# Kernel optimization log

Hardware: AMD Instinct MI355X
Metric: run time of the kernel (lower is better)

## Reference

```python
import jax, jax.numpy as jnp
import numpy as np


def setup_inputs() -> dict:
    key = jax.random.key(0)
    ks = jax.random.split(key, 7)
    T, B, I, H, O = 512, 64, 256, 512, 64
    std = 1.0 / np.sqrt(H)
    u = lambda k, shp: jax.random.uniform(k, shp, jnp.float32, -std, std)
    return {
        "x": jax.random.normal(ks[0], (T, B, I), jnp.float32),
        "x2h_w": u(ks[1], (3 * H, I)),
        "x2h_b": u(ks[2], (3 * H,)),
        "h2h_w": u(ks[3], (3 * H, H)),
        "h2h_b": u(ks[4], (3 * H,)),
        "fc_w": jax.random.normal(ks[5], (O, H), jnp.float32) * 0.05,
        "fc_b": jnp.zeros((O,), jnp.float32),
    }


def _gru_forward(x, x2h_w, x2h_b, h2h_w, h2h_b, fc_w, fc_b):
    T, B, _ = x.shape
    H = h2h_w.shape[1]
    # Precompute input projection for all timesteps: [T, B, 3H]
    x_proj = jnp.einsum("tbi,gi->tbg", x, x2h_w) + x2h_b

    def step(h, xp):
        h_t = h @ h2h_w.T + h2h_b  # [B, 3H]
        x_r, x_u, x_n = jnp.split(xp, 3, axis=1)
        h_r, h_u, h_n = jnp.split(h_t, 3, axis=1)
        reset = jax.nn.sigmoid(x_r + h_r)
        update = jax.nn.sigmoid(x_u + h_u)
        new = jnp.tanh(x_n + reset * h_n)
        hy = update * h + (1.0 - update) * new
        return hy, hy

    h0 = jnp.zeros((B, H), x.dtype)
    h_last, rnn_activity = jax.lax.scan(step, h0, x_proj)
    out = jnp.einsum("tbh,oh->tbo", rnn_activity, fc_w) + fc_b
    return out, rnn_activity


def reference(x, x2h_w, x2h_b, h2h_w, h2h_b, fc_w, fc_b):
    return _gru_forward(x, x2h_w, x2h_b, h2h_w, h2h_b, fc_w, fc_b)
```

## Files before the change

### kernel.cpp

```cpp
#include <hip/hip_runtime.h>
#include <cstdint>
#include <cstddef>

#define TT 512
#define BB 64
#define II 256
#define HH 512
#define GG 1536
#define OO 64
#define NWG 256
#define TAGPAD 16

__global__ __launch_bounds__(256)
void xproj_kernel(const float* __restrict__ x, const float* __restrict__ w,
                  const float* __restrict__ xb, float* __restrict__ xp)
{
    __shared__ float xs[64][68];
    __shared__ float ws[64][68];
    const int t  = blockIdx.y;
    const int g0 = blockIdx.x * 64;
    const int tid = threadIdx.x;
    const int gq = tid >> 4;
    const int bq = tid & 15;
    float acc[4][4];
#pragma unroll
    for (int j = 0; j < 4; ++j)
#pragma unroll
        for (int i = 0; i < 4; ++i) acc[j][i] = 0.f;

    for (int kc = 0; kc < 4; ++kc) {
        const int k0 = kc * 64;
        __syncthreads();
        for (int idx = tid; idx < 1024; idx += 256) {
            int r = idx >> 4, c4 = (idx & 15) * 4;
            float4 v = *(const float4*)(x + ((size_t)t * BB + r) * II + k0 + c4);
            xs[r][c4] = v.x; xs[r][c4+1] = v.y; xs[r][c4+2] = v.z; xs[r][c4+3] = v.w;
            float4 u = *(const float4*)(w + (size_t)(g0 + r) * II + k0 + c4);
            ws[r][c4] = u.x; ws[r][c4+1] = u.y; ws[r][c4+2] = u.z; ws[r][c4+3] = u.w;
        }
        __syncthreads();
#pragma unroll 4
        for (int k4 = 0; k4 < 16; ++k4) {
            float4 xv[4], wv[4];
#pragma unroll
            for (int i = 0; i < 4; ++i)
                xv[i] = *(const float4*)&xs[bq + 16*i][k4*4];
#pragma unroll
            for (int j = 0; j < 4; ++j)
                wv[j] = *(const float4*)&ws[gq + 16*j][k4*4];
#pragma unroll
            for (int j = 0; j < 4; ++j)
#pragma unroll
                for (int i = 0; i < 4; ++i) {
                    acc[j][i] = fmaf(wv[j].x, xv[i].x, acc[j][i]);
                    acc[j][i] = fmaf(wv[j].y, xv[i].y, acc[j][i]);
                    acc[j][i] = fmaf(wv[j].z, xv[i].z, acc[j][i]);
                    acc[j][i] = fmaf(wv[j].w, xv[i].w, acc[j][i]);
                }
        }
    }
#pragma unroll
    for (int j = 0; j < 4; ++j) {
        int g = g0 + gq + 16*j;
        float bg = xb[g];
#pragma unroll
        for (int i = 0; i < 4; ++i) {
            int b = bq + 16*i;
            xp[((size_t)t * GG + g) * BB + b] = acc[j][i] + bg;
        }
    }
}

__global__ __launch_bounds__(1024, 4)
void scan_kernel(const float* __restrict__ xp, const float* __restrict__ hw,
                 const float* __restrict__ hbias, float* __restrict__ rnn,
                 int* __restrict__ tags)
{
    __shared__ float hlds[8][512];
    __shared__ float pad_[17408];
    __shared__ int s_rk;

    const int tid = threadIdx.x;
    ((volatile float*)pad_)[tid] = 0.f;

    int xcc;
    asm volatile("s_getreg_b32 %0, hwreg(HW_REG_XCC_ID)" : "=s"(xcc));
    const int g = xcc & 7;
    if (tid == 0) {
        __threadfence();
        s_rk = atomicAdd(tags + (size_t)g * 32 * TAGPAD + 8, 1);
    }
    __syncthreads();
    const int rk = s_rk;
    if (rk >= 32) return;

    const int w    = tid >> 6;
    const int l    = tid & 63;
    const int cp   = w >> 1;
    const int bh   = w & 1;
    const int c0w  = rk * 16 + 2 * cp;
    const int col  = c0w + ((l >> 2) & 1);
    const int ob   = 8 * g + 4 * bh + (l & 3);

    const int sb = tid >> 7;
    const int sk = (tid & 127) * 4;

    float wreg[6][8];
#pragma unroll
    for (int rr = 0; rr < 6; ++rr) {
        const float* wp = hw + ((size_t)(rr >> 1) * HH + c0w + (rr & 1)) * HH;
        float4 a = *(const float4*)(wp + 4 * l);
        float4 b = *(const float4*)(wp + 256 + 4 * l);
        wreg[rr][0] = a.x; wreg[rr][1] = a.y; wreg[rr][2] = a.z; wreg[rr][3] = a.w;
        wreg[rr][4] = b.x; wreg[rr][5] = b.y; wreg[rr][6] = b.z; wreg[rr][7] = b.w;
    }
    const float bhr = hbias[col];
    const float bhu = hbias[HH + col];
    const float bhn = hbias[2 * HH + col];

    float hloc = 0.f;
    long long budget = 4000000;

    for (int t = 0; t < TT; ++t) {
        float xr = 0.f, xu = 0.f, xn = 0.f;
        if (l < 8) {
            const size_t xbase = (size_t)t * GG * BB;
            xr = xp[xbase + (size_t)(0 * HH + col) * BB + ob];
            xu = xp[xbase + (size_t)(1 * HH + col) * BB + ob];
            xn = xp[xbase + (size_t)(2 * HH + col) * BB + ob];
        }

        float g0v = 0.f, g1v = 0.f, g2v = 0.f;
        if (t > 0) {
            if (tid < 32) {
                const int* tp = tags + ((size_t)g * 32 + tid) * TAGPAD;
                int v;
                do {
                    asm volatile("global_load_dword %0, %1, off sc0 sc1\n\t"
                                 "s_waitcnt vmcnt(0)"
                                 : "=v"(v) : "v"(tp) : "memory");
                    if (v >= t) break;
                    __builtin_amdgcn_s_sleep(1);
                } while (--budget > 0);
            }
            __syncthreads();

            {
                const float* src = rnn + (size_t)(t - 1) * BB * HH
                                       + (size_t)(8 * g + sb) * HH + sk;
                *(float4*)&hlds[sb][sk] = *(const float4*)src;
            }
            __syncthreads();

            float acc[4][6];
#pragma unroll
            for (int bi = 0; bi < 4; ++bi) {
                float4 hA = *(const float4*)&hlds[4 * bh + bi][4 * l];
                float4 hB = *(const float4*)&hlds[4 * bh + bi][256 + 4 * l];
#pragma unroll
                for (int rr = 0; rr < 6; ++rr) {
                    float a;
                    a = hA.x * wreg[rr][0];
                    a = fmaf(hA.y, wreg[rr][1], a);
                    a = fmaf(hA.z, wreg[rr][2], a);
                    a = fmaf(hA.w, wreg[rr][3], a);
                    a = fmaf(hB.x, wreg[rr][4], a);
                    a = fmaf(hB.y, wreg[rr][5], a);
                    a = fmaf(hB.z, wreg[rr][6], a);
                    a = fmaf(hB.w, wreg[rr][7], a);
                    acc[bi][rr] = a;
                }
            }

            const int s0 = l & 1, s1 = (l >> 1) & 1, s2 = (l >> 2) & 1;
            float a1[2][6];
#pragma unroll
            for (int rr = 0; rr < 6; ++rr)
#pragma unroll
                for (int p = 0; p < 2; ++p) {
                    float lo = acc[2*p][rr], hi = acc[2*p+1][rr];
                    float send = s0 ? lo : hi;
                    float keep = s0 ? hi : lo;
                    a1[p][rr] = keep + __shfl_xor(send, 1, 64);
                }
            float a2[6];
#pragma unroll
            for (int rr = 0; rr < 6; ++rr) {
                float lo = a1[0][rr], hi = a1[1][rr];
                float send = s1 ? lo : hi;
                float keep = s1 ? hi : lo;
                a2[rr] = keep + __shfl_xor(send, 2, 64);
            }
            float a3[3];
#pragma unroll
            for (int gate = 0; gate < 3; ++gate) {
                float lo = a2[2*gate], hi = a2[2*gate + 1];
                float send = s2 ? lo : hi;
                float keep = s2 ? hi : lo;
                a3[gate] = keep + __shfl_xor(send, 4, 64);
            }
            g0v = a3[0]; g1v = a3[1]; g2v = a3[2];
            g0v += __shfl_xor(g0v, 8, 64); g0v += __shfl_xor(g0v, 16, 64); g0v += __shfl_xor(g0v, 32, 64);
            g1v += __shfl_xor(g1v, 8, 64); g1v += __shfl_xor(g1v, 16, 64); g1v += __shfl_xor(g1v, 32, 64);
            g2v += __shfl_xor(g2v, 8, 64); g2v += __shfl_xor(g2v, 16, 64); g2v += __shfl_xor(g2v, 32, 64);
        }

        if (l < 8) {
            float rg = 1.f / (1.f + __expf(-(xr + g0v + bhr)));
            float ug = 1.f / (1.f + __expf(-(xu + g1v + bhu)));
            float npre = xn + rg * (g2v + bhn);
            float e  = __expf(-2.f * npre);
            float nv = 2.f / (1.f + e) - 1.f;
            float hy = ug * hloc + (1.f - ug) * nv;
            hloc = hy;
            float* dst = rnn + ((size_t)t * BB + ob) * HH + col;
            asm volatile("global_store_dword %0, %1, off"
                         :: "v"(dst), "v"(hy) : "memory");
        }
        asm volatile("s_waitcnt vmcnt(0)" ::: "memory");
        __syncthreads();
        if (tid == 0) {
            int tv = t + 1;
            int* tp = tags + ((size_t)g * 32 + rk) * TAGPAD;
            asm volatile("global_store_dword %0, %1, off sc0 sc1"
                         :: "v"(tp), "v"(tv) : "memory");
        }
    }
}

__global__ __launch_bounds__(256)
void fc_kernel(const float* __restrict__ rnn, const float* __restrict__ fcw,
               const float* __restrict__ fcb, float* __restrict__ out)
{
    __shared__ float wlds[128][65];
    const int t = blockIdx.x;
    const int tid = threadIdx.x;
    const int o  = tid & 63;
    const int bg = tid >> 6;
    float acc[16];
#pragma unroll
    for (int i = 0; i < 16; ++i) acc[i] = 0.f;

    for (int kc = 0; kc < 4; ++kc) {
        const int k0 = kc * 128;
        __syncthreads();
        for (int idx = tid; idx < 64 * 32; idx += 256) {
            int oo = idx >> 5, kq = (idx & 31) * 4;
            float4 v = *(const float4*)(fcw + (size_t)oo * HH + k0 + kq);
            wlds[kq][oo] = v.x; wlds[kq+1][oo] = v.y;
            wlds[kq+2][oo] = v.z; wlds[kq+3][oo] = v.w;
        }
        __syncthreads();
#pragma unroll 2
        for (int k4 = 0; k4 < 32; ++k4) {
            float w0 = wlds[k4*4+0][o], w1 = wlds[k4*4+1][o];
            float w2 = wlds[k4*4+2][o], w3 = wlds[k4*4+3][o];
#pragma unroll
            for (int i = 0; i < 16; ++i) {
                int bb = bg * 16 + i;
                float4 h4 = *(const float4*)(rnn + ((size_t)t * BB + bb) * HH + k0 + k4*4);
                acc[i] = fmaf(h4.x, w0, fmaf(h4.y, w1, fmaf(h4.z, w2, fmaf(h4.w, w3, acc[i]))));
            }
        }
    }
    float bo = fcb[o];
#pragma unroll
    for (int i = 0; i < 16; ++i) {
        int bb = bg * 16 + i;
        out[((size_t)t * BB + bb) * OO + o] = acc[i] + bo;
    }
}

extern "C" void kernel_launch(void* const* d_in, const int* in_sizes, int n_in,
                              void* d_out, int out_size, void* d_ws, size_t ws_size,
                              hipStream_t stream)
{
    const float* x     = (const float*)d_in[0];
    const float* x2h_w = (const float*)d_in[1];
    const float* x2h_b = (const float*)d_in[2];
    const float* h2h_w = (const float*)d_in[3];
    const float* h2h_b = (const float*)d_in[4];
    const float* fc_w  = (const float*)d_in[5];
    const float* fc_b  = (const float*)d_in[6];

    float* out = (float*)d_out;
    float* rnn = (float*)d_out + (size_t)TT * BB * OO;

    float* xp = (float*)d_ws;
    const size_t xp_bytes = (size_t)TT * GG * BB * sizeof(float);
    int* tags = (int*)((char*)d_ws + xp_bytes);

    hipMemsetAsync(tags, 0, NWG * TAGPAD * sizeof(int), stream);

    dim3 gA(GG / 64, TT);
    xproj_kernel<<<gA, 256, 0, stream>>>(x, x2h_w, x2h_b, xp);
    scan_kernel<<<NWG, 1024, 0, stream>>>(xp, h2h_w, h2h_b, rnn, tags);
    fc_kernel<<<TT, 256, 0, stream>>>(rnn, fc_w, fc_b, out);
}
```

Before: 2.494 ms.

## Cut per-step barriers in GRU scan with double-buffered LDS and per-thread tag waits

The recurrent scan now double-buffers the hidden-state LDS tile. This removes one __syncthreads per timestep, and every thread polls the single producer tag that covers its own slice instead of 32 threads polling all tags. The end-of-step barrier is replaced by an LDS atomic counter, so the last wave to finish publishes the ready flag. The gate reduction is also rearranged by permuting the weight rows per lane, which removes the select-based shuffles, and pointer increments take over from index recomputation. This shortens the serial critical path of each timestep, at the cost of subtler memory-ordering correctness and more global polling traffic.

```diff
diff --git a/kernel.cpp b/kernel.cpp
--- a/kernel.cpp
+++ b/kernel.cpp
@@ -76,9 +76,10 @@
                  const float* __restrict__ hbias, float* __restrict__ rnn,
                  int* __restrict__ tags)
 {
-    __shared__ float hlds[8][512];
-    __shared__ float pad_[17408];
+    __shared__ float hlds[2][8][512];
+    __shared__ float pad_[12544];
     __shared__ int s_rk;
+    __shared__ int s_cnt;
 
     const int tid = threadIdx.x;
     ((volatile float*)pad_)[tid] = 0.f;
@@ -88,7 +89,8 @@
     const int g = xcc & 7;
     if (tid == 0) {
         __threadfence();
-        s_rk = atomicAdd(tags + (size_t)g * 32 * TAGPAD + 8, 1);
+        s_cnt = 0;
+        s_rk = atomicAdd(tags + NWG * TAGPAD + g * 16, 1);
     }
     __syncthreads();
     const int rk = s_rk;
@@ -99,16 +101,28 @@
     const int cp   = w >> 1;
     const int bh   = w & 1;
     const int c0w  = rk * 16 + 2 * cp;
-    const int col  = c0w + ((l >> 2) & 1);
+    const int s0 = l & 1, s1 = (l >> 1) & 1, s2 = (l >> 2) & 1;
+    const int col  = c0w + s2;
     const int ob   = 8 * g + 4 * bh + (l & 3);
 
     const int sb = tid >> 7;
     const int sk = (tid & 127) * 4;
+    const int soff = sb * 512 + sk;
+
+    const int* tp  = tags + ((size_t)g * 32 + (sk >> 4)) * TAGPAD;
+    int* tagme     = (int*)(tags + ((size_t)g * 32 + rk) * TAGPAD);
+
+    const int r0 = 2*s1 + s0, r1 = r0 ^ 2, r2 = r0 ^ 1, r3 = r0 ^ 3;
+    float* hflat = &hlds[0][0][0];
+    const int roff0 = (4*bh + r0) * 512 + 4*l;
+    const int roff1 = (4*bh + r1) * 512 + 4*l;
+    const int roff2 = (4*bh + r2) * 512 + 4*l;
+    const int roff3 = (4*bh + r3) * 512 + 4*l;
 
     float wreg[6][8];
 #pragma unroll
     for (int rr = 0; rr < 6; ++rr) {
-        const float* wp = hw + ((size_t)(rr >> 1) * HH + c0w + (rr & 1)) * HH;
+        const float* wp = hw + ((size_t)(rr >> 1) * HH + c0w + ((rr & 1) ^ s2)) * HH;
         float4 a = *(const float4*)(wp + 4 * l);
         float4 b = *(const float4*)(wp + 256 + 4 * l);
         wreg[rr][0] = a.x; wreg[rr][1] = a.y; wreg[rr][2] = a.z; wreg[rr][3] = a.w;
@@ -118,22 +132,22 @@
     const float bhu = hbias[HH + col];
     const float bhn = hbias[2 * HH + col];
 
+    const float* xpr = xp + (size_t)(0 * HH + col) * BB + ob;
+    const float* xpu = xp + (size_t)(1 * HH + col) * BB + ob;
+    const float* xpn = xp + (size_t)(2 * HH + col) * BB + ob;
+    const float* hsp = rnn + (size_t)(8 * g + sb) * HH + sk;
+    float*       dst = rnn + (size_t)ob * HH + col;
+
     float hloc = 0.f;
     long long budget = 4000000;
 
     for (int t = 0; t < TT; ++t) {
         float xr = 0.f, xu = 0.f, xn = 0.f;
-        if (l < 8) {
-            const size_t xbase = (size_t)t * GG * BB;
-            xr = xp[xbase + (size_t)(0 * HH + col) * BB + ob];
-            xu = xp[xbase + (size_t)(1 * HH + col) * BB + ob];
-            xn = xp[xbase + (size_t)(2 * HH + col) * BB + ob];
-        }
+        if (l < 8) { xr = *xpr; xu = *xpu; xn = *xpn; }
 
         float g0v = 0.f, g1v = 0.f, g2v = 0.f;
         if (t > 0) {
-            if (tid < 32) {
-                const int* tp = tags + ((size_t)g * 32 + tid) * TAGPAD;
+            {
                 int v;
                 do {
                     asm volatile("global_load_dword %0, %1, off sc0 sc1\n\t"
@@ -143,62 +157,60 @@
                     __builtin_amdgcn_s_sleep(1);
                 } while (--budget > 0);
             }
+            {
+                float4 hv = *(const float4*)hsp;
+                *(float4*)(hflat + (t & 1) * 4096 + soff) = hv;
+            }
+            hsp += BB * HH;
             __syncthreads();
 
-            {
-                const float* src = rnn + (size_t)(t - 1) * BB * HH
-                                       + (size_t)(8 * g + sb) * HH + sk;
-                *(float4*)&hlds[sb][sk] = *(const float4*)src;
-            }
-            __syncthreads();
-
-            float acc[4][6];
-#pragma unroll
-            for (int bi = 0; bi < 4; ++bi) {
-                float4 hA = *(const float4*)&hlds[4 * bh + bi][4 * l];
-                float4 hB = *(const float4*)&hlds[4 * bh + bi][256 + 4 * l];
-#pragma unroll
-                for (int rr = 0; rr < 6; ++rr) {
-                    float a;
-                    a = hA.x * wreg[rr][0];
-                    a = fmaf(hA.y, wreg[rr][1], a);
-                    a = fmaf(hA.z, wreg[rr][2], a);
-                    a = fmaf(hA.w, wreg[rr][3], a);
-                    a = fmaf(hB.x, wreg[rr][4], a);
-                    a = fmaf(hB.y, wreg[rr][5], a);
-                    a = fmaf(hB.z, wreg[rr][6], a);
-                    a = fmaf(hB.w, wreg[rr][7], a);
-                    acc[bi][rr] = a;
-                }
-            }
-
-            const int s0 = l & 1, s1 = (l >> 1) & 1, s2 = (l >> 2) & 1;
-            float a1[2][6];
+            const float* hb = hflat + (t & 1) * 4096;
+            float4 hA0 = *(const float4*)(hb + roff0), hB0 = *(const float4*)(hb + roff0 + 256);
+            float4 hA1 = *(const float4*)(hb + roff1), hB1 = *(const float4*)(hb + roff1 + 256);
+            float4 hA2 = *(const float4*)(hb + roff2), hB2 = *(const float4*)(hb + roff2 + 256);
+            float4 hA3 = *(const float4*)(hb + roff3), hB3 = *(const float4*)(hb + roff3 + 256);
+            float accA[6], accB[6], accC[6], accD[6];
+#pragma unroll
+            for (int rr = 0; rr < 6; ++rr) {
+                float a;
+                a = hA0.x * wreg[rr][0];
+                a = fmaf(hA0.y, wreg[rr][1], a); a = fmaf(hA0.z, wreg[rr][2], a);
+                a = fmaf(hA0.w, wreg[rr][3], a); a = fmaf(hB0.x, wreg[rr][4], a);
+                a = fmaf(hB0.y, wreg[rr][5], a); a = fmaf(hB0.z, wreg[rr][6], a);
+                a = fmaf(hB0.w, wreg[rr][7], a);
+                accA[rr] = a;
+                a = hA1.x * wreg[rr][0];
+                a = fmaf(hA1.y, wreg[rr][1], a); a = fmaf(hA1.z, wreg[rr][2], a);
+                a = fmaf(hA1.w, wreg[rr][3], a); a = fmaf(hB1.x, wreg[rr][4], a);
+                a = fmaf(hB1.y, wreg[rr][5], a); a = fmaf(hB1.z, wreg[rr][6], a);
+                a = fmaf(hB1.w, wreg[rr][7], a);
+                accB[rr] = a;
+                a = hA2.x * wreg[rr][0];
+                a = fmaf(hA2.y, wreg[rr][1], a); a = fmaf(hA2.z, wreg[rr][2], a);
+                a = fmaf(hA2.w, wreg[rr][3], a); a = fmaf(hB2.x, wreg[rr][4], a);
+                a = fmaf(hB2.y, wreg[rr][5], a); a = fmaf(hB2.z, wreg[rr][6], a);
+                a = fmaf(hB2.w, wreg[rr][7], a);
+                accC[rr] = a;
+                a = hA3.x * wreg[rr][0];
+                a = fmaf(hA3.y, wreg[rr][1], a); a = fmaf(hA3.z, wreg[rr][2], a);
+                a = fmaf(hA3.w, wreg[rr][3], a); a = fmaf(hB3.x, wreg[rr][4], a);
+                a = fmaf(hB3.y, wreg[rr][5], a); a = fmaf(hB3.z, wreg[rr][6], a);
+                a = fmaf(hB3.w, wreg[rr][7], a);
+                accD[rr] = a;
+            }
+
+            float t0[6], t1[6], a2[6], a3[3];
+#pragma unroll
+            for (int rr = 0; rr < 6; ++rr) {
+                t0[rr] = accA[rr] + __shfl_xor(accC[rr], 1, 64);
+                t1[rr] = accB[rr] + __shfl_xor(accD[rr], 1, 64);
+            }
 #pragma unroll
             for (int rr = 0; rr < 6; ++rr)
-#pragma unroll
-                for (int p = 0; p < 2; ++p) {
-                    float lo = acc[2*p][rr], hi = acc[2*p+1][rr];
-                    float send = s0 ? lo : hi;
-                    float keep = s0 ? hi : lo;
-                    a1[p][rr] = keep + __shfl_xor(send, 1, 64);
-                }
-            float a2[6];
-#pragma unroll
-            for (int rr = 0; rr < 6; ++rr) {
-                float lo = a1[0][rr], hi = a1[1][rr];
-                float send = s1 ? lo : hi;
-                float keep = s1 ? hi : lo;
-                a2[rr] = keep + __shfl_xor(send, 2, 64);
-            }
-            float a3[3];
-#pragma unroll
-            for (int gate = 0; gate < 3; ++gate) {
-                float lo = a2[2*gate], hi = a2[2*gate + 1];
-                float send = s2 ? lo : hi;
-                float keep = s2 ? hi : lo;
-                a3[gate] = keep + __shfl_xor(send, 4, 64);
-            }
+                a2[rr] = t0[rr] + __shfl_xor(t1[rr], 2, 64);
+#pragma unroll
+            for (int gt = 0; gt < 3; ++gt)
+                a3[gt] = a2[2*gt] + __shfl_xor(a2[2*gt + 1], 4, 64);
             g0v = a3[0]; g1v = a3[1]; g2v = a3[2];
             g0v += __shfl_xor(g0v, 8, 64); g0v += __shfl_xor(g0v, 16, 64); g0v += __shfl_xor(g0v, 32, 64);
             g1v += __shfl_xor(g1v, 8, 64); g1v += __shfl_xor(g1v, 16, 64); g1v += __shfl_xor(g1v, 32, 64);
@@ -213,18 +225,20 @@
             float nv = 2.f / (1.f + e) - 1.f;
             float hy = ug * hloc + (1.f - ug) * nv;
             hloc = hy;
-            float* dst = rnn + ((size_t)t * BB + ob) * HH + col;
             asm volatile("global_store_dword %0, %1, off"
                          :: "v"(dst), "v"(hy) : "memory");
         }
         asm volatile("s_waitcnt vmcnt(0)" ::: "memory");
-        __syncthreads();
-        if (tid == 0) {
-            int tv = t + 1;
-            int* tp = tags + ((size_t)g * 32 + rk) * TAGPAD;
-            asm volatile("global_store_dword %0, %1, off sc0 sc1"
-                         :: "v"(tp), "v"(tv) : "memory");
-        }
+        if (l == 0) {
+            int old = atomicAdd(&s_cnt, 1);
+            if (old == 16 * t + 15) {
+                int tv = t + 1;
+                asm volatile("global_store_dword %0, %1, off sc0 sc1"
+                             :: "v"(tagme), "v"(tv) : "memory");
+            }
+        }
+        xpr += GG * BB; xpu += GG * BB; xpn += GG * BB;
+        dst += BB * HH;
     }
 }
 
@@ -290,7 +304,7 @@
     const size_t xp_bytes = (size_t)TT * GG * BB * sizeof(float);
     int* tags = (int*)((char*)d_ws + xp_bytes);
 
-    hipMemsetAsync(tags, 0, NWG * TAGPAD * sizeof(int), stream);
+    hipMemsetAsync(tags, 0, (NWG * TAGPAD + 8 * 16) * sizeof(int), stream);
 
     dim3 gA(GG / 64, TT);
     xproj_kernel<<<gA, 256, 0, stream>>>(x, x2h_w, x2h_b, xp);
```

Measured after the change: 3.253 ms. +30.4%, slower.
